# Performance work log

Measured on AMD Instinct MI355X. Metric: run time of the kernel, lower is better.

## Reference

```python
import jax, jax.numpy as jnp
import numpy as np

B, N, DIM = 32, 1024, 768
H, S, D = 16, 4, 64  # num_heads, num_subheads (L=H*S=64), attn_dim


def setup_inputs() -> dict:
    key = jax.random.key(0)
    k1, k2, k3, k4 = jax.random.split(key, 4)
    x = jax.random.normal(k1, (B, N, DIM), dtype=jnp.float32)
    eos_indices = jax.random.randint(k2, (B,), 0, N)
    # q_emb: original shape (1,H,S,1,D); singleton dims dropped -> (H,S,D)
    q_emb = jax.random.normal(k3, (H, S, D), dtype=jnp.float32)
    # k Linear(dim -> H*D), xavier-uniform weight, zero bias (share_kv: v == k)
    limit = float(np.sqrt(6.0 / (DIM + H * D)))
    Wk = jax.random.uniform(k4, (DIM, H * D), dtype=jnp.float32, minval=-limit, maxval=limit)
    bk = jnp.zeros((H * D,), dtype=jnp.float32)
    return {"x": x, "eos_indices": eos_indices, "q_emb": q_emb, "Wk": Wk, "bk": bk}


def reference(x, eos_indices, q_emb, Wk, bk):
    # x: (B,N,dim); shared k/v projection -> (B,N,H,D)
    kv = (x @ Wk + bk).reshape(x.shape[0], x.shape[1], H, D)
    scale = D ** -0.5
    # Avoid the torch expand over subheads: contract directly.
    # logits: (B,H,S,N)
    logits = jnp.einsum("hsd,bnhd->bhsn", q_emb * scale, kv)
    # eos masking: positions strictly after eos index are masked out
    mask = jnp.arange(x.shape[1])[None, None, None, :] > eos_indices[:, None, None, None]
    logits = jnp.where(mask, -jnp.inf, logits)
    attn = jax.nn.softmax(logits, axis=-1)
    # weighted sum over N -> (B,H,S,D) -> (B,L,D)
    out = jnp.einsum("bhsn,bnhd->bhsd", attn, kv)
    return out.reshape(x.shape[0], H * S, D)
```

## Files before the change

### kernel.cpp

```cpp
#include <hip/hip_runtime.h>
#include <hip/hip_bf16.h>
#include <stdint.h>

typedef float  f32x4  __attribute__((ext_vector_type(4)));
typedef __bf16 bf16x4 __attribute__((ext_vector_type(4)));
typedef __bf16 bf16x8 __attribute__((ext_vector_type(8)));
typedef unsigned int u32x2 __attribute__((ext_vector_type(2)));
typedef unsigned int u32x4 __attribute__((ext_vector_type(4)));

#define AS1 __attribute__((address_space(1)))
#define AS3 __attribute__((address_space(3)))

__device__ __forceinline__ void async_load16(const void* g, void* lds) {
    __builtin_amdgcn_global_load_lds((const AS1 unsigned int*)g,
                                     (AS3 unsigned int*)lds, 16, 0, 0);
}

__global__ __launch_bounds__(256) void qw_kernel(const float* __restrict__ q_emb,
                                                 const float* __restrict__ wk,
                                                 __bf16* __restrict__ qwT) {
    __shared__ float qlds[256];
    __shared__ float part[4096];
    const int t = threadIdx.x;
    const int kc = blockIdx.x;
    const int h  = blockIdx.y;
    const int k0 = kc * 64;
    qlds[t] = q_emb[h * 256 + t] * 0.125f;
    __syncthreads();
    const int dseg = t & 15;
    const int krow = t >> 4;
#pragma unroll
    for (int i = 0; i < 4; ++i) {
        const int k = i * 16 + krow;
        f32x4 wv = *(const f32x4*)&wk[(size_t)(k0 + k) * 1024 + h * 64 + dseg * 4];
#pragma unroll
        for (int s = 0; s < 4; ++s) {
            float p = qlds[s * 64 + dseg * 4 + 0] * wv[0]
                    + qlds[s * 64 + dseg * 4 + 1] * wv[1]
                    + qlds[s * 64 + dseg * 4 + 2] * wv[2]
                    + qlds[s * 64 + dseg * 4 + 3] * wv[3];
            part[k * 64 + s * 16 + dseg] = p;
        }
    }
    __syncthreads();
    const int k = t >> 2, s = t & 3;
    const float* pp = &part[k * 64 + s * 16];
    float sum = 0.f;
#pragma unroll
    for (int j = 0; j < 16; ++j) sum += pp[j];
    qwT[(h * 4 + s) * 768 + k0 + k] = (__bf16)sum;
}

__global__ __launch_bounds__(512) void logits_kernel(const float* __restrict__ x,
                                                     const __bf16* __restrict__ qwT,
                                                     const int* __restrict__ eos_idx,
                                                     __bf16* __restrict__ Lg,
                                                     float* __restrict__ partials) {
    __shared__ char smem[49152];
    char* Bl = smem;
    char* Al = smem + 16384;
    const int t = threadIdx.x, l = t & 63, w = t >> 6;
    const int m0 = blockIdx.x * 128;
    const int bb = m0 >> 10, n0 = m0 & 1023;
    const int chunk = blockIdx.x & 7;
    const int wrA = (w >> 1) * 32;
    const int wcB = (w & 1) * 32;

    f32x4 acc[2][2];
#pragma unroll
    for (int i = 0; i < 2; ++i)
#pragma unroll
        for (int j = 0; j < 2; ++j) acc[i][j] = (f32x4)0.f;

    const int Bcol = t >> 3, Bseg = t & 7;
    const __bf16* qsrc = qwT + Bcol * 768 + (Bseg ^ (Bcol & 7)) * 8;
    const int Arow0 = t >> 4;
    const int Aseg = t & 15;

    f32x4 av[4];
    async_load16(qsrc, Bl + t * 16);
#pragma unroll
    for (int i = 0; i < 4; ++i)
        av[i] = *(const f32x4*)&x[(size_t)(m0 + i * 32 + Arow0) * 768 + Aseg * 4];
#pragma unroll
    for (int i = 0; i < 4; ++i) {
        const int row = i * 32 + Arow0;
        bf16x4 vv = {(__bf16)av[i][0], (__bf16)av[i][1], (__bf16)av[i][2], (__bf16)av[i][3]};
        *(bf16x4*)(Al + ((row * 128 + Aseg * 8) ^ ((row & 7) << 4))) = vv;
    }
    asm volatile("s_waitcnt vmcnt(0)" ::: "memory");
    __syncthreads();

    int buf = 0;
    for (int step = 0; step < 12; ++step) {
        const int nbuf = buf ^ 1;
        const bool more = (step + 1) < 12;
        if (more) {
            const int kt = (step + 1) * 64;
            async_load16(qsrc + kt, Bl + nbuf * 8192 + t * 16);
#pragma unroll
            for (int i = 0; i < 4; ++i)
                av[i] = *(const f32x4*)&x[(size_t)(m0 + i * 32 + Arow0) * 768 + kt + Aseg * 4];
        }
#pragma unroll
        for (int kh = 0; kh < 2; ++kh) {
            const int u = kh * 4 + (l >> 4);
            bf16x8 af[2], bfr[2];
#pragma unroll
            for (int i = 0; i < 2; ++i) {
                const int row = wrA + i * 16 + (l & 15);
                af[i] = *(const bf16x8*)(Al + buf * 16384 +
                                         ((row * 128 + u * 16) ^ ((row & 7) << 4)));
            }
#pragma unroll
            for (int j = 0; j < 2; ++j) {
                const int col = wcB + j * 16 + (l & 15);
                bfr[j] = *(const bf16x8*)(Bl + buf * 8192 +
                                          ((col * 128 + u * 16) ^ ((col & 7) << 4)));
            }
#pragma unroll
            for (int i = 0; i < 2; ++i)
#pragma unroll
                for (int j = 0; j < 2; ++j)
                    acc[i][j] = __builtin_amdgcn_mfma_f32_16x16x32_bf16(
                        af[i], bfr[j], acc[i][j], 0, 0, 0);
        }
        if (more) {
#pragma unroll
            for (int i = 0; i < 4; ++i) {
                const int row = i * 32 + Arow0;
                bf16x4 vv = {(__bf16)av[i][0], (__bf16)av[i][1], (__bf16)av[i][2], (__bf16)av[i][3]};
                *(bf16x4*)(Al + nbuf * 16384 + ((row * 128 + Aseg * 8) ^ ((row & 7) << 4))) = vv;
            }
        }
        asm volatile("s_waitcnt vmcnt(0)" ::: "memory");
        __syncthreads();
        buf = nbuf;
    }

#pragma unroll
    for (int i = 0; i < 2; ++i)
#pragma unroll
        for (int j = 0; j < 2; ++j) {
            const int hs = wcB + j * 16 + (l & 15);
            const int nb = wrA + i * 16 + (l >> 4) * 4;
            *(f32x4*)(smem + ((hs * 512 + nb * 4) ^ ((hs & 7) << 4))) = acc[i][j];
        }
    __syncthreads();
    const int eosb = eos_idx[bb];
    const int hs = t >> 3, seg7 = t & 7;
    const int fH = (hs & 7) << 4;
    float mx = -INFINITY;
    bf16x4 pk4[4];
#pragma unroll
    for (int i = 0; i < 4; ++i) {
        const int seg = seg7 + i * 8;
        f32x4 v = *(const f32x4*)(smem + ((hs * 512 + seg * 16) ^ fH));
        bf16x4 pk;
#pragma unroll
        for (int j = 0; j < 4; ++j) {
            const float f = (n0 + seg * 4 + j > eosb) ? -INFINITY : v[j];
            pk[j] = (__bf16)f;
            mx = fmaxf(mx, (float)pk[j]);
        }
        pk4[i] = pk;
        *(bf16x4*)&Lg[(size_t)bb * 65536 + hs * 1024 + n0 + seg * 4] = pk;
    }
#pragma unroll
    for (int off = 1; off < 8; off <<= 1) mx = fmaxf(mx, __shfl_xor(mx, off));
    float sl = 0.f;
    if (mx > -INFINITY) {
#pragma unroll
        for (int i = 0; i < 4; ++i)
#pragma unroll
            for (int j = 0; j < 4; ++j) sl += __expf((float)pk4[i][j] - mx);
    }
#pragma unroll
    for (int off = 1; off < 8; off <<= 1) sl += __shfl_xor(sl, off);
    if (seg7 == 0) {
        float2 st = {mx, sl};
        *(float2*)&partials[(size_t)(((bb * 8 + chunk) * 64) + hs) * 2] = st;
    }
}

__global__ __launch_bounds__(256, 3) void pv_kernel(const float* __restrict__ x,
                                                    const __bf16* __restrict__ Lg,
                                                    const float* __restrict__ partials,
                                                    float* __restrict__ y) {
    __shared__ char smem[32768];
    char* Pl = smem;
    char* Xl = smem + 16384;
    const int t = threadIdx.x, l = t & 63, w = t >> 6;
    const int vid = (blockIdx.x & 7) * 48 + (blockIdx.x >> 3);
    const int b = vid / 12, kc = vid % 12;
    const int k0 = kc * 64;
    const int wrA = (w >> 1) * 32, wcB = (w & 1) * 32;
    const __bf16* Lgb = Lg + (size_t)b * 65536;
    const float* xb = x + (size_t)b * 786432 + k0 + l;
    const int fK = ((l & 7) << 4) | (((l >> 3) & 1) << 3);

    const int r0 = t >> 3, r1 = 32 + (t >> 3);
    float m0r, i0r, m1r, i1r;
    {
        const float* pb = partials + (size_t)b * 1024;
        float m = -INFINITY, m2 = -INFINITY;
#pragma unroll
        for (int c = 0; c < 8; ++c) {
            m  = fmaxf(m,  pb[(c * 64 + r0) * 2]);
            m2 = fmaxf(m2, pb[(c * 64 + r1) * 2]);
        }
        float s = 0.f, s2 = 0.f;
#pragma unroll
        for (int c = 0; c < 8; ++c) {
            float2 p0 = *(const float2*)&pb[(c * 64 + r0) * 2];
            float2 p1 = *(const float2*)&pb[(c * 64 + r1) * 2];
            s  += p0.y * __expf(p0.x - m);
            s2 += p1.y * __expf(p1.x - m2);
        }
        m0r = m; i0r = 1.0f / s;
        m1r = m2; i1r = 1.0f / s2;
    }
    const int n0s0 = (((t & 7) ^ (r0 & 7)) * 8);
    const int n0s1 = (((t & 7) ^ (r1 & 7)) * 8);

    f32x4 acc[2][2];
#pragma unroll
    for (int i = 0; i < 2; ++i)
#pragma unroll
        for (int j = 0; j < 2; ++j) acc[i][j] = (f32x4)0.f;

    auto STAGE = [&](int bufb, int T) {
        bf16x8 g0 = *(const bf16x8*)&Lgb[(size_t)r0 * 1024 + T * 64 + n0s0];
        bf16x8 g1 = *(const bf16x8*)&Lgb[(size_t)r1 * 1024 + T * 64 + n0s1];
        float xv[16];
#pragma unroll
        for (int i_ = 0; i_ < 4; ++i_)
#pragma unroll
            for (int j_ = 0; j_ < 4; ++j_)
                xv[i_ * 4 + j_] = xb[(size_t)(T * 64 + i_ * 16 + w * 4 + j_) * 768];
        bf16x8 pk;
#pragma unroll
        for (int j_ = 0; j_ < 8; ++j_)
            pk[j_] = (__bf16)(__expf((float)g0[j_] - m0r) * i0r);
        *(bf16x8*)(Pl + bufb * 8192 + t * 16) = pk;
#pragma unroll
        for (int j_ = 0; j_ < 8; ++j_)
            pk[j_] = (__bf16)(__expf((float)g1[j_] - m1r) * i1r);
        *(bf16x8*)(Pl + bufb * 8192 + 4096 + t * 16) = pk;
#pragma unroll
        for (int i_ = 0; i_ < 4; ++i_) {
            bf16x4 vv = {(__bf16)xv[i_ * 4 + 0], (__bf16)xv[i_ * 4 + 1],
                         (__bf16)xv[i_ * 4 + 2], (__bf16)xv[i_ * 4 + 3]};
            *(bf16x4*)(Xl + bufb * 8192 + ((l * 128 + (i_ * 16 + w * 4) * 2) ^ fK)) = vv;
        }
    };
    auto COMPUTE = [&](int bufb) {
#pragma unroll
        for (int kh = 0; kh < 2; ++kh) {
            const int u = kh * 4 + (l >> 4);
            bf16x8 af[2], bfr[2];
#pragma unroll
            for (int i = 0; i < 2; ++i) {
                const int row = wrA + i * 16 + (l & 15);
                af[i] = *(const bf16x8*)(Pl + bufb * 8192 +
                                         ((row * 128 + u * 16) ^ ((row & 7) << 4)));
            }
#pragma unroll
            for (int j = 0; j < 2; ++j) {
                const int kcol = wcB + j * 16 + (l & 15);
                const int fKc = ((kcol & 7) << 4) | (((kcol >> 3) & 1) << 3);
                const int addrA = kcol * 128 + kh * 64 + (l >> 4) * 16;
                u32x2 lo = *(const u32x2*)(Xl + bufb * 8192 + (addrA ^ fKc));
                u32x2 hi = *(const u32x2*)(Xl + bufb * 8192 + ((addrA + 8) ^ fKc));
                u32x4 uu = {lo[0], lo[1], hi[0], hi[1]};
                bfr[j] = __builtin_bit_cast(bf16x8, uu);
            }
#pragma unroll
            for (int i = 0; i < 2; ++i)
#pragma unroll
                for (int j = 0; j < 2; ++j)
                    acc[i][j] = __builtin_amdgcn_mfma_f32_16x16x32_bf16(
                        af[i], bfr[j], acc[i][j], 0, 0, 0);
        }
    };

    STAGE(0, 0);
    __syncthreads();
    int buf = 0;
    for (int step = 0; step < 16; ++step) {
        if (step + 1 < 16) STAGE(buf ^ 1, step + 1);
        COMPUTE(buf);
        __syncthreads();
        buf ^= 1;
    }

#pragma unroll
    for (int i = 0; i < 2; ++i)
#pragma unroll
        for (int j = 0; j < 2; ++j) {
            const int kcol = wcB + j * 16 + (l & 15);
#pragma unroll
            for (int r = 0; r < 4; ++r) {
                const int hs2 = wrA + i * 16 + (l >> 4) * 4 + r;
                *(float*)(smem + ((hs2 * 256 + kcol * 4) ^ ((hs2 & 7) << 4))) = acc[i][j][r];
            }
        }
    __syncthreads();
    const int hs2 = t >> 2;
#pragma unroll
    for (int i = 0; i < 4; ++i) {
        const int seg = (t & 3) + i * 4;
        f32x4 v = *(const f32x4*)(smem + ((hs2 * 256 + seg * 16) ^ ((hs2 & 7) << 4)));
        *(f32x4*)&y[(size_t)(b * 64 + hs2) * 768 + k0 + seg * 4] = v;
    }
}

__global__ __launch_bounds__(256) void out_kernel(const float* __restrict__ y,
                                                  const float* __restrict__ wk,
                                                  const float* __restrict__ bk,
                                                  float* __restrict__ out) {
    __shared__ float ylds[8 * 768];
    __shared__ float red[2048];
    const int t = threadIdx.x;
    const int vid = (blockIdx.x & 7) * 32 + (blockIdx.x >> 3);
    const int h = vid >> 4, bp = vid & 15;
#pragma unroll
    for (int r = 0; r < 8; ++r) {
        const int gb = bp * 2 + (r >> 2);
        const int hs = h * 4 + (r & 3);
#pragma unroll
        for (int i = 0; i < 3; ++i)
            ylds[r * 768 + i * 256 + t] = y[(size_t)(gb * 64 + hs) * 768 + i * 256 + t];
    }
    __syncthreads();
    const int kp = t >> 6, d = t & 63;
    float acc[8] = {0.f, 0.f, 0.f, 0.f, 0.f, 0.f, 0.f, 0.f};
    for (int i = 0; i < 48; ++i) {
        const int k = kp * 192 + i * 4;
        const float wv0 = wk[(size_t)(k + 0) * 1024 + h * 64 + d];
        const float wv1 = wk[(size_t)(k + 1) * 1024 + h * 64 + d];
        const float wv2 = wk[(size_t)(k + 2) * 1024 + h * 64 + d];
        const float wv3 = wk[(size_t)(k + 3) * 1024 + h * 64 + d];
#pragma unroll
        for (int r = 0; r < 8; ++r) {
            f32x4 yv = *(const f32x4*)&ylds[r * 768 + k];
            acc[r] += yv[0] * wv0 + yv[1] * wv1 + yv[2] * wv2 + yv[3] * wv3;
        }
    }
#pragma unroll
    for (int r = 0; r < 8; ++r) red[(r * 64 + d) * 4 + kp] = acc[r];
    __syncthreads();
#pragma unroll
    for (int i = 0; i < 2; ++i) {
        const int o = i * 256 + t;
        const int r = o >> 6, dd = o & 63;
        f32x4 pv = *(const f32x4*)&red[o * 4];
        const float s = pv[0] + pv[1] + pv[2] + pv[3] + bk[h * 64 + dd];
        const int gb = bp * 2 + (r >> 2);
        out[(size_t)(gb * 64 + h * 4 + (r & 3)) * 64 + dd] = s;
    }
}

extern "C" void kernel_launch(void* const* d_in, const int* in_sizes, int n_in,
                              void* d_out, int out_size, void* d_ws, size_t ws_size,
                              hipStream_t stream) {
    const float* x     = (const float*)d_in[0];
    const int*   eos   = (const int*)d_in[1];
    const float* q_emb = (const float*)d_in[2];
    const float* Wk    = (const float*)d_in[3];
    const float* bk    = (const float*)d_in[4];
    float* out = (float*)d_out;

    char* ws = (char*)d_ws;
    __bf16* qwT      = (__bf16*)ws;
    __bf16* Lg       = (__bf16*)(ws + 131072);
    float*  partials = (float*)(ws + 4325376);
    float*  y        = (float*)(ws + 4456448);

    qw_kernel<<<dim3(12, 16), 256, 0, stream>>>(q_emb, Wk, qwT);
    logits_kernel<<<dim3(256), 512, 0, stream>>>(x, qwT, eos, Lg, partials);
    pv_kernel<<<dim3(384), 256, 0, stream>>>(x, Lg, partials, y);
    out_kernel<<<dim3(256), 256, 0, stream>>>(y, Wk, bk, out);
}
```

Before: 63.76 us.

## Preload full qW matrix into LDS and stream x directly into MFMA registers

The qw kernel now writes qwT in a pre-swizzled layout, so the logits kernel can copy the whole 64x768 bf16 qW matrix into 96KB of LDS with a few async loads up front. The per-step double-buffered LDS staging of x and the per-step barriers are removed. Each lane instead loads its own x fragments from global memory into registers, converts them to bf16 in place and feeds MFMA, with ping-pong register buffers hiding load latency. This removes LDS round trips and syncs for A, at the cost of more LDS per block (lower occupancy), more registers, and possibly duplicated x loads across the two column-warps.

Result: slower. 70.00 us (+9.8%).

```diff
diff --git a/kernel.cpp b/kernel.cpp
--- a/kernel.cpp
+++ b/kernel.cpp
@@ -48,7 +48,8 @@
     float sum = 0.f;
 #pragma unroll
     for (int j = 0; j < 16; ++j) sum += pp[j];
-    qwT[(h * 4 + s) * 768 + k0 + k] = (__bf16)sum;
+    const int row = h * 4 + s;
+    qwT[row * 768 + ((k0 + k) ^ ((row & 7) << 3))] = (__bf16)sum;
 }
 
 __global__ __launch_bounds__(512) void logits_kernel(const float* __restrict__ x,
@@ -56,9 +57,7 @@
                                                      const int* __restrict__ eos_idx,
                                                      __bf16* __restrict__ Lg,
                                                      float* __restrict__ partials) {
-    __shared__ char smem[49152];
-    char* Bl = smem;
-    char* Al = smem + 16384;
+    __shared__ char smem[98304];
     const int t = threadIdx.x, l = t & 63, w = t >> 6;
     const int m0 = blockIdx.x * 128;
     const int bb = m0 >> 10, n0 = m0 & 1023;
@@ -66,77 +65,66 @@
     const int wrA = (w >> 1) * 32;
     const int wcB = (w & 1) * 32;
 
+#pragma unroll
+    for (int c = 0; c < 12; ++c)
+        async_load16((const char*)qwT + c * 8192 + t * 16, smem + c * 8192 + t * 16);
+
+    const int arow0 = m0 + wrA + (l & 15);
+    const int kslot = (l >> 4) * 8;
+
     f32x4 acc[2][2];
 #pragma unroll
     for (int i = 0; i < 2; ++i)
 #pragma unroll
         for (int j = 0; j < 2; ++j) acc[i][j] = (f32x4)0.f;
 
-    const int Bcol = t >> 3, Bseg = t & 7;
-    const __bf16* qsrc = qwT + Bcol * 768 + (Bseg ^ (Bcol & 7)) * 8;
-    const int Arow0 = t >> 4;
-    const int Aseg = t & 15;
-
-    f32x4 av[4];
-    async_load16(qsrc, Bl + t * 16);
-#pragma unroll
-    for (int i = 0; i < 4; ++i)
-        av[i] = *(const f32x4*)&x[(size_t)(m0 + i * 32 + Arow0) * 768 + Aseg * 4];
-#pragma unroll
-    for (int i = 0; i < 4; ++i) {
-        const int row = i * 32 + Arow0;
-        bf16x4 vv = {(__bf16)av[i][0], (__bf16)av[i][1], (__bf16)av[i][2], (__bf16)av[i][3]};
-        *(bf16x4*)(Al + ((row * 128 + Aseg * 8) ^ ((row & 7) << 4))) = vv;
-    }
-    asm volatile("s_waitcnt vmcnt(0)" ::: "memory");
-    __syncthreads();
-
-    int buf = 0;
-    for (int step = 0; step < 12; ++step) {
-        const int nbuf = buf ^ 1;
-        const bool more = (step + 1) < 12;
-        if (more) {
-            const int kt = (step + 1) * 64;
-            async_load16(qsrc + kt, Bl + nbuf * 8192 + t * 16);
-#pragma unroll
-            for (int i = 0; i < 4; ++i)
-                av[i] = *(const f32x4*)&x[(size_t)(m0 + i * 32 + Arow0) * 768 + kt + Aseg * 4];
-        }
+    f32x4 aLo[4], aHi[4], bLo[4], bHi[4];
+
+    auto LOADA = [&](f32x4* lo, f32x4* hi, int kt) {
+#pragma unroll
+        for (int i = 0; i < 2; ++i)
+#pragma unroll
+            for (int kh = 0; kh < 2; ++kh) {
+                const float* p = &x[(size_t)(arow0 + i * 16) * 768 + kt + kh * 32 + kslot];
+                lo[i * 2 + kh] = *(const f32x4*)p;
+                hi[i * 2 + kh] = *(const f32x4*)(p + 4);
+            }
+    };
+    auto COMP = [&](const f32x4* lo, const f32x4* hi, int step) {
 #pragma unroll
         for (int kh = 0; kh < 2; ++kh) {
-            const int u = kh * 4 + (l >> 4);
-            bf16x8 af[2], bfr[2];
-#pragma unroll
-            for (int i = 0; i < 2; ++i) {
-                const int row = wrA + i * 16 + (l & 15);
-                af[i] = *(const bf16x8*)(Al + buf * 16384 +
-                                         ((row * 128 + u * 16) ^ ((row & 7) << 4)));
-            }
+            const int kk2 = (step * 64 + kh * 32 + kslot) * 2;
+            bf16x8 bfr[2];
 #pragma unroll
             for (int j = 0; j < 2; ++j) {
                 const int col = wcB + j * 16 + (l & 15);
-                bfr[j] = *(const bf16x8*)(Bl + buf * 8192 +
-                                          ((col * 128 + u * 16) ^ ((col & 7) << 4)));
-            }
-#pragma unroll
-            for (int i = 0; i < 2; ++i)
+                bfr[j] = *(const bf16x8*)(smem + ((col * 1536 + kk2) ^ ((col & 7) << 4)));
+            }
+#pragma unroll
+            for (int i = 0; i < 2; ++i) {
+                f32x4 L = lo[i * 2 + kh], H = hi[i * 2 + kh];
+                bf16x8 af = {(__bf16)L[0], (__bf16)L[1], (__bf16)L[2], (__bf16)L[3],
+                             (__bf16)H[0], (__bf16)H[1], (__bf16)H[2], (__bf16)H[3]};
 #pragma unroll
                 for (int j = 0; j < 2; ++j)
                     acc[i][j] = __builtin_amdgcn_mfma_f32_16x16x32_bf16(
-                        af[i], bfr[j], acc[i][j], 0, 0, 0);
-        }
-        if (more) {
-#pragma unroll
-            for (int i = 0; i < 4; ++i) {
-                const int row = i * 32 + Arow0;
-                bf16x4 vv = {(__bf16)av[i][0], (__bf16)av[i][1], (__bf16)av[i][2], (__bf16)av[i][3]};
-                *(bf16x4*)(Al + nbuf * 16384 + ((row * 128 + Aseg * 8) ^ ((row & 7) << 4))) = vv;
-            }
-        }
-        asm volatile("s_waitcnt vmcnt(0)" ::: "memory");
-        __syncthreads();
-        buf = nbuf;
-    }
+                        af, bfr[j], acc[i][j], 0, 0, 0);
+            }
+        }
+    };
+
+    LOADA(aLo, aHi, 0);
+    asm volatile("s_waitcnt vmcnt(0)" ::: "memory");
+    __syncthreads();
+
+#pragma unroll
+    for (int it = 0; it < 6; ++it) {
+        LOADA(bLo, bHi, (2 * it + 1) * 64);
+        COMP(aLo, aHi, 2 * it);
+        if (it < 5) LOADA(aLo, aHi, (2 * it + 2) * 64);
+        COMP(bLo, bHi, 2 * it + 1);
+    }
+    __syncthreads();
 
 #pragma unroll
     for (int i = 0; i < 2; ++i)
```

## Fuse logits and PV into per-chunk flash-style kernel with eos chunk skipping

Applied to the files above, without the earlier changes.

Replaces the separate logits and PV kernels with one kernel per 64-token chunk. Each chunk computes its logits, a local softmax, and a partial P·X product for all 12 K-slices, and writes unnormalized bf16 partials. A new combine kernel rescales and sums those partials using the per-chunk max and sum. Chunks lying wholly past the eos index exit early, which skips masked work. The price is a large bf16 partial buffer (about 50MB) that must be written and read back, which could outweigh the savings from fewer x reads and skipped chunks.

Result: no change. 63.60 us (-0.2%).

```diff
diff --git a/kernel.cpp b/kernel.cpp
--- a/kernel.cpp
+++ b/kernel.cpp
@@ -51,18 +51,25 @@
     qwT[(h * 4 + s) * 768 + k0 + k] = (__bf16)sum;
 }
 
-__global__ __launch_bounds__(512) void logits_kernel(const float* __restrict__ x,
-                                                     const __bf16* __restrict__ qwT,
-                                                     const int* __restrict__ eos_idx,
-                                                     __bf16* __restrict__ Lg,
-                                                     float* __restrict__ partials) {
-    __shared__ char smem[49152];
-    char* Bl = smem;
-    char* Al = smem + 16384;
+__global__ __launch_bounds__(256) void fused_chunk(const float* __restrict__ x,
+                                                   const __bf16* __restrict__ qwT,
+                                                   const int* __restrict__ eos_idx,
+                                                   float* __restrict__ partials,
+                                                   __bf16* __restrict__ u) {
+    __shared__ char smem[32768];
+    char* R0 = smem;
+    char* R1 = smem + 16384;
     const int t = threadIdx.x, l = t & 63, w = t >> 6;
-    const int m0 = blockIdx.x * 128;
-    const int bb = m0 >> 10, n0 = m0 & 1023;
-    const int chunk = blockIdx.x & 7;
+    const int vid = ((blockIdx.x & 7) << 6) + (blockIdx.x >> 3);
+    const int b = vid >> 4, c = vid & 15;
+    const int eosb = eos_idx[b];
+    float* pb = partials + ((size_t)(b * 16 + c) * 64) * 2;
+
+    if (c * 64 > eosb) {
+        if (t < 64) { pb[t * 2] = -INFINITY; pb[t * 2 + 1] = 0.f; }
+        return;
+    }
+
     const int wrA = (w >> 1) * 32;
     const int wcB = (w & 1) * 32;
 
@@ -72,21 +79,29 @@
 #pragma unroll
         for (int j = 0; j < 2; ++j) acc[i][j] = (f32x4)0.f;
 
-    const int Bcol = t >> 3, Bseg = t & 7;
-    const __bf16* qsrc = qwT + Bcol * 768 + (Bseg ^ (Bcol & 7)) * 8;
-    const int Arow0 = t >> 4;
-    const int Aseg = t & 15;
-
-    f32x4 av[4];
-    async_load16(qsrc, Bl + t * 16);
-#pragma unroll
-    for (int i = 0; i < 4; ++i)
-        av[i] = *(const f32x4*)&x[(size_t)(m0 + i * 32 + Arow0) * 768 + Aseg * 4];
-#pragma unroll
-    for (int i = 0; i < 4; ++i) {
-        const int row = i * 32 + Arow0;
-        bf16x4 vv = {(__bf16)av[i][0], (__bf16)av[i][1], (__bf16)av[i][2], (__bf16)av[i][3]};
-        *(bf16x4*)(Al + ((row * 128 + Aseg * 8) ^ ((row & 7) << 4))) = vv;
+    const int qcol = t >> 3, qseg = t & 7;
+    const __bf16* qsrc0 = qwT + qcol * 768 + ((qseg ^ (qcol & 7)) * 8);
+    const __bf16* qsrc1 = qsrc0 + 32 * 768;
+    const int xr = t >> 2, xseg = (t & 3) * 16;
+    const float* xrow = &x[(size_t)(b * 1024 + c * 64 + xr) * 768 + xseg];
+    const int fR = (xr & 7) << 4;
+    const int Adst0 = (xr * 128 + xseg * 2) ^ fR;
+    const int Adst1 = (xr * 128 + xseg * 2 + 16) ^ fR;
+
+    f32x4 xv0, xv1, xv2, xv3;
+    async_load16(qsrc0, R0 + t * 16);
+    async_load16(qsrc1, R0 + 4096 + t * 16);
+    xv0 = *(const f32x4*)(xrow);
+    xv1 = *(const f32x4*)(xrow + 4);
+    xv2 = *(const f32x4*)(xrow + 8);
+    xv3 = *(const f32x4*)(xrow + 12);
+    {
+        bf16x8 v0 = {(__bf16)xv0[0], (__bf16)xv0[1], (__bf16)xv0[2], (__bf16)xv0[3],
+                     (__bf16)xv1[0], (__bf16)xv1[1], (__bf16)xv1[2], (__bf16)xv1[3]};
+        bf16x8 v1 = {(__bf16)xv2[0], (__bf16)xv2[1], (__bf16)xv2[2], (__bf16)xv2[3],
+                     (__bf16)xv3[0], (__bf16)xv3[1], (__bf16)xv3[2], (__bf16)xv3[3]};
+        *(bf16x8*)(R1 + Adst0) = v0;
+        *(bf16x8*)(R1 + Adst1) = v1;
     }
     asm volatile("s_waitcnt vmcnt(0)" ::: "memory");
     __syncthreads();
@@ -97,26 +112,28 @@
         const bool more = (step + 1) < 12;
         if (more) {
             const int kt = (step + 1) * 64;
-            async_load16(qsrc + kt, Bl + nbuf * 8192 + t * 16);
-#pragma unroll
-            for (int i = 0; i < 4; ++i)
-                av[i] = *(const f32x4*)&x[(size_t)(m0 + i * 32 + Arow0) * 768 + kt + Aseg * 4];
+            async_load16(qsrc0 + kt, R0 + nbuf * 8192 + t * 16);
+            async_load16(qsrc1 + kt, R0 + nbuf * 8192 + 4096 + t * 16);
+            xv0 = *(const f32x4*)(xrow + kt);
+            xv1 = *(const f32x4*)(xrow + kt + 4);
+            xv2 = *(const f32x4*)(xrow + kt + 8);
+            xv3 = *(const f32x4*)(xrow + kt + 12);
         }
 #pragma unroll
         for (int kh = 0; kh < 2; ++kh) {
-            const int u = kh * 4 + (l >> 4);
+            const int koff = (kh * 32 + (l >> 4) * 8) * 2;
             bf16x8 af[2], bfr[2];
 #pragma unroll
             for (int i = 0; i < 2; ++i) {
                 const int row = wrA + i * 16 + (l & 15);
-                af[i] = *(const bf16x8*)(Al + buf * 16384 +
-                                         ((row * 128 + u * 16) ^ ((row & 7) << 4)));
+                af[i] = *(const bf16x8*)(R1 + buf * 8192 +
+                                         ((row * 128 + koff) ^ ((row & 7) << 4)));
             }
 #pragma unroll
             for (int j = 0; j < 2; ++j) {
                 const int col = wcB + j * 16 + (l & 15);
-                bfr[j] = *(const bf16x8*)(Bl + buf * 8192 +
-                                          ((col * 128 + u * 16) ^ ((col & 7) << 4)));
+                bfr[j] = *(const bf16x8*)(R0 + buf * 8192 +
+                                          ((col * 128 + koff) ^ ((col & 7) << 4)));
             }
 #pragma unroll
             for (int i = 0; i < 2; ++i)
@@ -126,12 +143,12 @@
                         af[i], bfr[j], acc[i][j], 0, 0, 0);
         }
         if (more) {
-#pragma unroll
-            for (int i = 0; i < 4; ++i) {
-                const int row = i * 32 + Arow0;
-                bf16x4 vv = {(__bf16)av[i][0], (__bf16)av[i][1], (__bf16)av[i][2], (__bf16)av[i][3]};
-                *(bf16x4*)(Al + nbuf * 16384 + ((row * 128 + Aseg * 8) ^ ((row & 7) << 4))) = vv;
-            }
+            bf16x8 v0 = {(__bf16)xv0[0], (__bf16)xv0[1], (__bf16)xv0[2], (__bf16)xv0[3],
+                         (__bf16)xv1[0], (__bf16)xv1[1], (__bf16)xv1[2], (__bf16)xv1[3]};
+            bf16x8 v1 = {(__bf16)xv2[0], (__bf16)xv2[1], (__bf16)xv2[2], (__bf16)xv2[3],
+                         (__bf16)xv3[0], (__bf16)xv3[1], (__bf16)xv3[2], (__bf16)xv3[3]};
+            *(bf16x8*)(R1 + nbuf * 8192 + Adst0) = v0;
+            *(bf16x8*)(R1 + nbuf * 8192 + Adst1) = v1;
         }
         asm volatile("s_waitcnt vmcnt(0)" ::: "memory");
         __syncthreads();
@@ -143,135 +160,94 @@
 #pragma unroll
         for (int j = 0; j < 2; ++j) {
             const int hs = wcB + j * 16 + (l & 15);
-            const int nb = wrA + i * 16 + (l >> 4) * 4;
-            *(f32x4*)(smem + ((hs * 512 + nb * 4) ^ ((hs & 7) << 4))) = acc[i][j];
-        }
-    __syncthreads();
-    const int eosb = eos_idx[bb];
-    const int hs = t >> 3, seg7 = t & 7;
-    const int fH = (hs & 7) << 4;
-    float mx = -INFINITY;
-    bf16x4 pk4[4];
-#pragma unroll
-    for (int i = 0; i < 4; ++i) {
-        const int seg = seg7 + i * 8;
-        f32x4 v = *(const f32x4*)(smem + ((hs * 512 + seg * 16) ^ fH));
-        bf16x4 pk;
-#pragma unroll
-        for (int j = 0; j < 4; ++j) {
-            const float f = (n0 + seg * 4 + j > eosb) ? -INFINITY : v[j];
-            pk[j] = (__bf16)f;
-            mx = fmaxf(mx, (float)pk[j]);
-        }
-        pk4[i] = pk;
-        *(bf16x4*)&Lg[(size_t)bb * 65536 + hs * 1024 + n0 + seg * 4] = pk;
-    }
-#pragma unroll
-    for (int off = 1; off < 8; off <<= 1) mx = fmaxf(mx, __shfl_xor(mx, off));
-    float sl = 0.f;
-    if (mx > -INFINITY) {
-#pragma unroll
-        for (int i = 0; i < 4; ++i)
-#pragma unroll
-            for (int j = 0; j < 4; ++j) sl += __expf((float)pk4[i][j] - mx);
-    }
-#pragma unroll
-    for (int off = 1; off < 8; off <<= 1) sl += __shfl_xor(sl, off);
-    if (seg7 == 0) {
-        float2 st = {mx, sl};
-        *(float2*)&partials[(size_t)(((bb * 8 + chunk) * 64) + hs) * 2] = st;
-    }
-}
-
-__global__ __launch_bounds__(256, 3) void pv_kernel(const float* __restrict__ x,
-                                                    const __bf16* __restrict__ Lg,
-                                                    const float* __restrict__ partials,
-                                                    float* __restrict__ y) {
-    __shared__ char smem[32768];
-    char* Pl = smem;
-    char* Xl = smem + 16384;
-    const int t = threadIdx.x, l = t & 63, w = t >> 6;
-    const int vid = (blockIdx.x & 7) * 48 + (blockIdx.x >> 3);
-    const int b = vid / 12, kc = vid % 12;
-    const int k0 = kc * 64;
-    const int wrA = (w >> 1) * 32, wcB = (w & 1) * 32;
-    const __bf16* Lgb = Lg + (size_t)b * 65536;
-    const float* xb = x + (size_t)b * 786432 + k0 + l;
+            const int n4 = wrA + i * 16 + (l >> 4) * 4;
+            *(f32x4*)(R0 + ((hs * 256 + n4 * 4) ^ ((hs & 7) << 4))) = acc[i][j];
+        }
+    __syncthreads();
+
+    {
+        const int hs = t >> 2, sg = t & 3;
+        const int fH = (hs & 7) << 4;
+        f32x4 v[4];
+        float mx = -INFINITY;
+#pragma unroll
+        for (int q = 0; q < 4; ++q) {
+            const int n = sg * 16 + q * 4;
+            f32x4 vv = *(const f32x4*)(R0 + ((hs * 256 + n * 4) ^ fH));
+#pragma unroll
+            for (int e = 0; e < 4; ++e) {
+                if (c * 64 + n + e > eosb) vv[e] = -INFINITY;
+                mx = fmaxf(mx, vv[e]);
+            }
+            v[q] = vv;
+        }
+#pragma unroll
+        for (int off = 1; off < 4; off <<= 1) mx = fmaxf(mx, __shfl_xor(mx, off));
+        float sl = 0.f;
+#pragma unroll
+        for (int q = 0; q < 4; ++q)
+#pragma unroll
+            for (int e = 0; e < 4; ++e) sl += __expf(v[q][e] - mx);
+#pragma unroll
+        for (int off = 1; off < 4; off <<= 1) sl += __shfl_xor(sl, off);
+        if (sg == 0) { pb[hs * 2] = mx; pb[hs * 2 + 1] = sl; }
+        bf16x8 p0, p1;
+#pragma unroll
+        for (int e = 0; e < 4; ++e) {
+            p0[e]     = (__bf16)__expf(v[0][e] - mx);
+            p0[4 + e] = (__bf16)__expf(v[1][e] - mx);
+            p1[e]     = (__bf16)__expf(v[2][e] - mx);
+            p1[4 + e] = (__bf16)__expf(v[3][e] - mx);
+        }
+        *(bf16x8*)(R1 + ((hs * 128 + sg * 32) ^ fH)) = p0;
+        *(bf16x8*)(R1 + ((hs * 128 + sg * 32 + 16) ^ fH)) = p1;
+    }
+    __syncthreads();
+
+    const float* xcb = x + (size_t)(b * 1024 + c * 64) * 768 + l;
     const int fK = ((l & 7) << 4) | (((l >> 3) & 1) << 3);
 
-    const int r0 = t >> 3, r1 = 32 + (t >> 3);
-    float m0r, i0r, m1r, i1r;
-    {
-        const float* pb = partials + (size_t)b * 1024;
-        float m = -INFINITY, m2 = -INFINITY;
-#pragma unroll
-        for (int c = 0; c < 8; ++c) {
-            m  = fmaxf(m,  pb[(c * 64 + r0) * 2]);
-            m2 = fmaxf(m2, pb[(c * 64 + r1) * 2]);
-        }
-        float s = 0.f, s2 = 0.f;
-#pragma unroll
-        for (int c = 0; c < 8; ++c) {
-            float2 p0 = *(const float2*)&pb[(c * 64 + r0) * 2];
-            float2 p1 = *(const float2*)&pb[(c * 64 + r1) * 2];
-            s  += p0.y * __expf(p0.x - m);
-            s2 += p1.y * __expf(p1.x - m2);
-        }
-        m0r = m; i0r = 1.0f / s;
-        m1r = m2; i1r = 1.0f / s2;
-    }
-    const int n0s0 = (((t & 7) ^ (r0 & 7)) * 8);
-    const int n0s1 = (((t & 7) ^ (r1 & 7)) * 8);
-
-    f32x4 acc[2][2];
-#pragma unroll
-    for (int i = 0; i < 2; ++i)
-#pragma unroll
-        for (int j = 0; j < 2; ++j) acc[i][j] = (f32x4)0.f;
-
-    auto STAGE = [&](int bufb, int T) {
-        bf16x8 g0 = *(const bf16x8*)&Lgb[(size_t)r0 * 1024 + T * 64 + n0s0];
-        bf16x8 g1 = *(const bf16x8*)&Lgb[(size_t)r1 * 1024 + T * 64 + n0s1];
+    auto STAGE = [&](int bufb, int kc) {
         float xv[16];
 #pragma unroll
         for (int i_ = 0; i_ < 4; ++i_)
 #pragma unroll
             for (int j_ = 0; j_ < 4; ++j_)
-                xv[i_ * 4 + j_] = xb[(size_t)(T * 64 + i_ * 16 + w * 4 + j_) * 768];
-        bf16x8 pk;
-#pragma unroll
-        for (int j_ = 0; j_ < 8; ++j_)
-            pk[j_] = (__bf16)(__expf((float)g0[j_] - m0r) * i0r);
-        *(bf16x8*)(Pl + bufb * 8192 + t * 16) = pk;
-#pragma unroll
-        for (int j_ = 0; j_ < 8; ++j_)
-            pk[j_] = (__bf16)(__expf((float)g1[j_] - m1r) * i1r);
-        *(bf16x8*)(Pl + bufb * 8192 + 4096 + t * 16) = pk;
+                xv[i_ * 4 + j_] = xcb[(size_t)(i_ * 16 + w * 4 + j_) * 768 + kc * 64];
 #pragma unroll
         for (int i_ = 0; i_ < 4; ++i_) {
             bf16x4 vv = {(__bf16)xv[i_ * 4 + 0], (__bf16)xv[i_ * 4 + 1],
                          (__bf16)xv[i_ * 4 + 2], (__bf16)xv[i_ * 4 + 3]};
-            *(bf16x4*)(Xl + bufb * 8192 + ((l * 128 + (i_ * 16 + w * 4) * 2) ^ fK)) = vv;
+            *(bf16x4*)(R0 + bufb * 8192 + ((l * 128 + (i_ * 16 + w * 4) * 2) ^ fK)) = vv;
         }
     };
-    auto COMPUTE = [&](int bufb) {
+
+    f32x4 acc2[2][2];
+    STAGE(0, 0);
+    __syncthreads();
+    int bufb = 0;
+    for (int kc = 0; kc < 12; ++kc) {
+        if (kc + 1 < 12) STAGE(bufb ^ 1, kc + 1);
+#pragma unroll
+        for (int i = 0; i < 2; ++i)
+#pragma unroll
+            for (int j = 0; j < 2; ++j) acc2[i][j] = (f32x4)0.f;
 #pragma unroll
         for (int kh = 0; kh < 2; ++kh) {
-            const int u = kh * 4 + (l >> 4);
+            const int u8 = kh * 4 + (l >> 4);
             bf16x8 af[2], bfr[2];
 #pragma unroll
             for (int i = 0; i < 2; ++i) {
                 const int row = wrA + i * 16 + (l & 15);
-                af[i] = *(const bf16x8*)(Pl + bufb * 8192 +
-                                         ((row * 128 + u * 16) ^ ((row & 7) << 4)));
+                af[i] = *(const bf16x8*)(R1 + ((row * 128 + u8 * 16) ^ ((row & 7) << 4)));
             }
 #pragma unroll
             for (int j = 0; j < 2; ++j) {
                 const int kcol = wcB + j * 16 + (l & 15);
                 const int fKc = ((kcol & 7) << 4) | (((kcol >> 3) & 1) << 3);
                 const int addrA = kcol * 128 + kh * 64 + (l >> 4) * 16;
-                u32x2 lo = *(const u32x2*)(Xl + bufb * 8192 + (addrA ^ fKc));
-                u32x2 hi = *(const u32x2*)(Xl + bufb * 8192 + ((addrA + 8) ^ fKc));
+                u32x2 lo = *(const u32x2*)(R0 + bufb * 8192 + (addrA ^ fKc));
+                u32x2 hi = *(const u32x2*)(R0 + bufb * 8192 + ((addrA + 8) ^ fKc));
                 u32x4 uu = {lo[0], lo[1], hi[0], hi[1]};
                 bfr[j] = __builtin_bit_cast(bf16x8, uu);
             }
@@ -279,19 +255,73 @@
             for (int i = 0; i < 2; ++i)
 #pragma unroll
                 for (int j = 0; j < 2; ++j)
-                    acc[i][j] = __builtin_amdgcn_mfma_f32_16x16x32_bf16(
-                        af[i], bfr[j], acc[i][j], 0, 0, 0);
-        }
-    };
-
-    STAGE(0, 0);
-    __syncthreads();
-    int buf = 0;
-    for (int step = 0; step < 16; ++step) {
-        if (step + 1 < 16) STAGE(buf ^ 1, step + 1);
-        COMPUTE(buf);
+                    acc2[i][j] = __builtin_amdgcn_mfma_f32_16x16x32_bf16(
+                        af[i], bfr[j], acc2[i][j], 0, 0, 0);
+        }
+        {
+            const size_t fb = (((size_t)(b * 16 + c) * 12 + kc) * 4 + w) * 4;
+#pragma unroll
+            for (int i = 0; i < 2; ++i)
+#pragma unroll
+                for (int j = 0; j < 2; ++j) {
+                    bf16x4 uv = {(__bf16)acc2[i][j][0], (__bf16)acc2[i][j][1],
+                                 (__bf16)acc2[i][j][2], (__bf16)acc2[i][j][3]};
+                    *(bf16x4*)&u[(fb + i * 2 + j) * 256 + l * 4] = uv;
+                }
+        }
         __syncthreads();
-        buf ^= 1;
+        bufb ^= 1;
+    }
+}
+
+__global__ __launch_bounds__(256) void combine_kernel(const float* __restrict__ partials,
+                                                      const __bf16* __restrict__ u,
+                                                      const int* __restrict__ eos_idx,
+                                                      float* __restrict__ y) {
+    __shared__ char smem[16384];
+    __shared__ float wgt[16 * 64];
+    const int t = threadIdx.x, l = t & 63, w = t >> 6;
+    const int vid = (blockIdx.x & 7) * 48 + (blockIdx.x >> 3);
+    const int b = vid / 12, kc = vid % 12;
+    const int nact = (eos_idx[b] >> 6) + 1;
+
+    if (t < 64) {
+        const float* pbb = partials + (size_t)b * 2048;
+        float M = -INFINITY;
+        for (int c = 0; c < nact; ++c) M = fmaxf(M, pbb[(c * 64 + t) * 2]);
+        float S = 0.f;
+        for (int c = 0; c < nact; ++c) {
+            float2 p = *(const float2*)&pbb[(c * 64 + t) * 2];
+            S += __expf(p.x - M) * p.y;
+        }
+        const float inv = 1.0f / S;
+        for (int c = 0; c < nact; ++c)
+            wgt[c * 64 + t] = __expf(pbb[(c * 64 + t) * 2] - M) * inv;
+    }
+    __syncthreads();
+
+    const int wrA = (w >> 1) * 32, wcB = (w & 1) * 32;
+    f32x4 yf[2][2];
+#pragma unroll
+    for (int i = 0; i < 2; ++i)
+#pragma unroll
+        for (int j = 0; j < 2; ++j) yf[i][j] = (f32x4)0.f;
+
+    for (int c = 0; c < nact; ++c) {
+        const size_t fb = (((size_t)(b * 16 + c) * 12 + kc) * 4 + w) * 4;
+        f32x4 wv[2];
+#pragma unroll
+        for (int i = 0; i < 2; ++i)
+            wv[i] = *(const f32x4*)&wgt[c * 64 + wrA + i * 16 + (l >> 4) * 4];
+#pragma unroll
+        for (int i = 0; i < 2; ++i)
+#pragma unroll
+            for (int j = 0; j < 2; ++j) {
+                bf16x4 uv = *(const bf16x4*)&u[(fb + i * 2 + j) * 256 + l * 4];
+#pragma unroll
+                for (int r = 0; r < 4; ++r)
+                    yf[i][j][r] += wv[i][r] * (float)uv[r];
+            }
     }
 
 #pragma unroll
@@ -302,7 +332,7 @@
 #pragma unroll
             for (int r = 0; r < 4; ++r) {
                 const int hs2 = wrA + i * 16 + (l >> 4) * 4 + r;
-                *(float*)(smem + ((hs2 * 256 + kcol * 4) ^ ((hs2 & 7) << 4))) = acc[i][j][r];
+                *(float*)(smem + ((hs2 * 256 + kcol * 4) ^ ((hs2 & 7) << 4))) = yf[i][j][r];
             }
         }
     __syncthreads();
@@ -311,7 +341,7 @@
     for (int i = 0; i < 4; ++i) {
         const int seg = (t & 3) + i * 4;
         f32x4 v = *(const f32x4*)(smem + ((hs2 * 256 + seg * 16) ^ ((hs2 & 7) << 4)));
-        *(f32x4*)&y[(size_t)(b * 64 + hs2) * 768 + k0 + seg * 4] = v;
+        *(f32x4*)&y[(size_t)(b * 64 + hs2) * 768 + kc * 64 + seg * 4] = v;
     }
 }
 
@@ -373,12 +403,12 @@
 
     char* ws = (char*)d_ws;
     __bf16* qwT      = (__bf16*)ws;
-    __bf16* Lg       = (__bf16*)(ws + 131072);
-    float*  partials = (float*)(ws + 4325376);
-    float*  y        = (float*)(ws + 4456448);
+    float*  partials = (float*)(ws + 131072);
+    __bf16* u        = (__bf16*)(ws + 393216);
+    float*  y        = (float*)(ws + 393216 + 50331648);
 
     qw_kernel<<<dim3(12, 16), 256, 0, stream>>>(q_emb, Wk, qwT);
-    logits_kernel<<<dim3(256), 512, 0, stream>>>(x, qwT, eos, Lg, partials);
-    pv_kernel<<<dim3(384), 256, 0, stream>>>(x, Lg, partials, y);
+    fused_chunk<<<dim3(512), 256, 0, stream>>>(x, qwT, eos, partials, u);
+    combine_kernel<<<dim3(384), 256, 0, stream>>>(partials, u, eos, y);
     out_kernel<<<dim3(256), 256, 0, stream>>>(y, Wk, bk, out);
 }
```
